# Kernel optimization log

Measured on AMD Instinct MI355X. Metric: run time of the kernel, lower is better.

Reference implementation:

```python
import jax, jax.numpy as jnp
import numpy as np

NW, NT = 200000, 100000
DW, DT = 128, 64
HID, HEADS, OUT = 64, 2, 2
HC = HID * HEADS  # 128
E = 500000
NEG_SLOPE = 0.2


def setup_inputs() -> dict:
    key = jax.random.key(0)
    ks = iter(jax.random.split(key, 40))

    def nrm(shape, scale):
        return jax.random.normal(next(ks), shape, dtype=jnp.float32) * scale

    inp = {
        "x_wallet": nrm((NW, DW), 1.0),
        "x_token": nrm((NT, DT), 1.0),
        # per-node-type input projections Linear(in, hidden)
        "lin_w_W": nrm((DW, HID), 1.0 / np.sqrt(DW)),
        "lin_w_b": jnp.zeros((HID,), jnp.float32),
        "lin_t_W": nrm((DT, HID), 1.0 / np.sqrt(DT)),
        "lin_t_b": jnp.zeros((HID,), jnp.float32),
        # GAT layer 0: in=HID(64) -> H*C(128), stacked over 3 edge types
        "Wsrc0": nrm((3, HID, HC), 1.0 / np.sqrt(HID)),
        "Wdst0": nrm((3, HID, HC), 1.0 / np.sqrt(HID)),
        "atts0": nrm((3, HEADS, HID), 1.0 / np.sqrt(HID)),
        "attd0": nrm((3, HEADS, HID), 1.0 / np.sqrt(HID)),
        "b0": jnp.zeros((3, HC), jnp.float32),
        # GAT layer 1: in=H*C(128) -> H*C(128)
        "Wsrc1": nrm((3, HC, HC), 1.0 / np.sqrt(HC)),
        "Wdst1": nrm((3, HC, HC), 1.0 / np.sqrt(HC)),
        "atts1": nrm((3, HEADS, HID), 1.0 / np.sqrt(HID)),
        "attd1": nrm((3, HEADS, HID), 1.0 / np.sqrt(HID)),
        "b1": jnp.zeros((3, HC), jnp.float32),
        # classifiers Linear(H*C, out)
        "cls_w_W": nrm((HC, OUT), 1.0 / np.sqrt(HC)),
        "cls_w_b": jnp.zeros((OUT,), jnp.float32),
        "cls_t_W": nrm((HC, OUT), 1.0 / np.sqrt(HC)),
        "cls_t_b": jnp.zeros((OUT,), jnp.float32),
        # edge indices: [2, E] with row0 = src ids, row1 = dst ids
        "e_wt": jnp.stack([jax.random.randint(next(ks), (E,), 0, NW),
                            jax.random.randint(next(ks), (E,), 0, NT)]).astype(jnp.int64),
        "e_tw": jnp.stack([jax.random.randint(next(ks), (E,), 0, NT),
                            jax.random.randint(next(ks), (E,), 0, NW)]).astype(jnp.int64),
        "e_ww": jnp.stack([jax.random.randint(next(ks), (E,), 0, NW),
                            jax.random.randint(next(ks), (E,), 0, NW)]).astype(jnp.int64),
    }
    return inp


def gat_conv(x_src, x_dst, edge, Wsrc, Wdst, att_s, att_d, bias, n_dst):
    # bipartite GATConv: project, per-edge attention, segment softmax over dst, scatter-sum
    hs = (x_src @ Wsrc).reshape(-1, HEADS, HID)  # [Ns,H,C]
    hd = (x_dst @ Wdst).reshape(-1, HEADS, HID)  # [Nd,H,C]
    a_s = jnp.einsum("nhc,hc->nh", hs, att_s)    # [Ns,H]
    a_d = jnp.einsum("nhc,hc->nh", hd, att_d)    # [Nd,H]
    s, d = edge[0], edge[1]
    alpha = jax.nn.leaky_relu(a_s[s] + a_d[d], NEG_SLOPE)  # [E,H]
    m = jax.ops.segment_max(alpha, d, num_segments=n_dst)
    m = jnp.where(jnp.isfinite(m), m, 0.0)  # nodes with no in-edges
    ex = jnp.exp(alpha - m[d])
    den = jax.ops.segment_sum(ex, d, num_segments=n_dst)
    alpha = ex / (den[d] + 1e-16)
    out = jax.ops.segment_sum(alpha[:, :, None] * hs[s], d, num_segments=n_dst)  # [Nd,H,C]
    return out.reshape(n_dst, HC) + bias


def reference(x_wallet, x_token, lin_w_W, lin_w_b, lin_t_W, lin_t_b,
              Wsrc0, Wdst0, atts0, attd0, b0,
              Wsrc1, Wdst1, atts1, attd1, b1,
              cls_w_W, cls_w_b, cls_t_W, cls_t_b,
              e_wt, e_tw, e_ww):
    xw = x_wallet @ lin_w_W + lin_w_b
    xt = x_token @ lin_t_W + lin_t_b
    for Wsrc, Wdst, ats, atd, b in ((Wsrc0, Wdst0, atts0, attd0, b0),
                                     (Wsrc1, Wdst1, atts1, attd1, b1)):
        # edge type 0: wallet->token, 1: token->wallet, 2: wallet->wallet; HeteroConv aggr='sum'
        out_t = gat_conv(xw, xt, e_wt, Wsrc[0], Wdst[0], ats[0], atd[0], b[0], NT)
        out_w = (gat_conv(xt, xw, e_tw, Wsrc[1], Wdst[1], ats[1], atd[1], b[1], NW)
                 + gat_conv(xw, xw, e_ww, Wsrc[2], Wdst[2], ats[2], atd[2], b[2], NW))
        xw = jax.nn.elu(out_w)
        xt = jax.nn.elu(out_t)
    logits_w = xw @ cls_w_W + cls_w_b  # [NW,2]
    logits_t = xt @ cls_t_W + cls_t_b  # [NT,2]
    return jnp.concatenate([logits_w, logits_t], axis=0)  # [NW+NT,2]
```

## Files before the change

kernel.cpp:

```cpp
#include <hip/hip_runtime.h>
#include <stdint.h>

typedef unsigned short ushort_t;
typedef short s8v __attribute__((ext_vector_type(8)));
typedef float f4v __attribute__((ext_vector_type(4)));

#define NW 200000
#define NT 100000
#define EE 500000
#define NSEG (NT + NW + NW)

__device__ __forceinline__ float b2f(unsigned short u){
  union { unsigned int i; float f; } v; v.i = ((unsigned int)u) << 16; return v.f;
}
__device__ __forceinline__ unsigned short f2b(float f){
  unsigned int x = __float_as_uint(f);
  unsigned int r = x + 0x7fffu + ((x >> 16) & 1u);
  return (unsigned short)(r >> 16);
}
__device__ __forceinline__ float ldf(const void* p, long idx, int fm){
  return fm ? ((const float*)p)[idx] : b2f(((const ushort_t*)p)[idx]);
}

__global__ void detect_kern(const int* ewt, const int* etw, const int* eww,
                            const unsigned* xw_words, int* mode){
  if (threadIdx.x == 0 && blockIdx.x == 0){
    unsigned o = 0;
    for (int i = 0; i < 64; ++i)
      o |= (unsigned)ewt[2 * i + 1] | (unsigned)etw[2 * i + 1] | (unsigned)eww[2 * i + 1];
    mode[0] = (o == 0) ? 1 : 0;
    int viol = 0;
    for (int i = 0; i < 256; ++i){
      unsigned s = xw_words[i] & 0xffffu;
      unsigned e = (s >> 7) & 0xffu;
      if (!(s == 0u || s == 0x8000u || (e >= 90u && e <= 140u))) viol++;
    }
    mode[1] = (viol > 8) ? 1 : 0;
  }
}

struct TDesc { const void* src; ushort_t* dst; long ebase; int K; int N; };
struct TDesc8 { TDesc d[8]; };
__global__ void transpose8(TDesc8 td, const int* mode){
  int fm = mode[1];
  int mi = blockIdx.x >> 6;
  TDesc t = td.d[mi];
  int e = ((blockIdx.x & 63) << 8) + threadIdx.x;
  if (e < t.K * t.N){
    int k = e / t.N, n = e - k * t.N;
    t.dst[n * t.K + k] = f2b(ldf(t.src, t.ebase + e, fm));
  }
}

__global__ void uprep(const void* Wsrc0, const void* Wdst0, const void* atts0, const void* attd0,
                      const void* Wsrc1, const void* Wdst1, const void* atts1, const void* attd1,
                      float* Uw0, float* Ut0, float* Uw1, float* Ut1, const int* mode){
  int fm = mode[1];
  int id = blockIdx.x * 256 + threadIdx.x;
  if (id >= (64 + 128) * 12) return;
  int layer = (id >= 64 * 12);
  int rem = layer ? id - 64 * 12 : id;
  int K = layer ? 128 : 64;
  int k = rem / 12, j = rem % 12;
  const void* Ws = layer ? Wsrc1 : Wsrc0;
  const void* Wd = layer ? Wdst1 : Wdst0;
  const void* As = layer ? atts1 : atts0;
  const void* Ad = layer ? attd1 : attd0;
  int t, h; bool src;
  if (j < 8){ const int tt[8] = {0,0,2,2,1,1,2,2}; t = tt[j]; h = j & 1; src = (j < 4); }
  else { int jj = j - 8; t = (jj < 2) ? 1 : 0; h = jj & 1; src = (jj < 2); }
  const void* W = src ? Ws : Wd;
  const void* A = src ? As : Ad;
  float acc = 0.f;
  for (int c = 0; c < 64; ++c)
    acc += ldf(W, (long)(t * K + k) * 128 + h * 64 + c, fm) * ldf(A, t * 128 + h * 64 + c, fm);
  if (j < 8) (layer ? Uw1 : Uw0)[k * 8 + j] = acc;
  else       (layer ? Ut1 : Ut0)[k * 4 + (j - 8)] = acc;
}

__global__ void hist_kern(const int* ewt, const int* etw, const int* eww, const int* mode, int* deg){
  int i = blockIdx.x * 256 + threadIdx.x;
  if (i >= 3 * EE) return;
  int md = mode[0];
  int t = i / EE, e = i - t * EE;
  const int* ep = (t == 0) ? ewt : (t == 1) ? etw : eww;
  int d = md ? ep[2 * (EE + e)] : ep[EE + e];
  int base = (t == 0) ? 0 : (t == 1) ? NT : NT + NW;
  atomicAdd(&deg[base + d], 1);
}

__global__ __launch_bounds__(512) void scan1(const int* deg, int* excl, int* sums){
  __shared__ int pair[512];
  int t = threadIdx.x;
  int base = blockIdx.x * 1024;
  int i0 = base + 2 * t;
  int a = (i0 < NSEG) ? deg[i0] : 0;
  int b = (i0 + 1 < NSEG) ? deg[i0 + 1] : 0;
  int ps = a + b;
  pair[t] = ps;
  __syncthreads();
  for (int off = 1; off < 512; off <<= 1){
    int v = (t >= off) ? pair[t - off] : 0;
    __syncthreads();
    if (t >= off) pair[t] += v;
    __syncthreads();
  }
  int epair = pair[t] - ps;
  if (i0 < NSEG) excl[i0] = epair;
  if (i0 + 1 < NSEG) excl[i0 + 1] = epair + a;
  if (t == 511) sums[blockIdx.x] = pair[511];
}

__global__ __launch_bounds__(512) void scan2(int* sums, int nch){
  __shared__ int s[512];
  int t = threadIdx.x;
  int orig = (t < nch) ? sums[t] : 0;
  s[t] = orig;
  __syncthreads();
  for (int off = 1; off < 512; off <<= 1){
    int v = (t >= off) ? s[t - off] : 0;
    __syncthreads();
    if (t >= off) s[t] += v;
    __syncthreads();
  }
  if (t < nch) sums[t] = s[t] - orig;
}

__global__ void scan3(int* rowptr, int* cursor, const int* sums){
  int i = blockIdx.x * 256 + threadIdx.x;
  if (i < NSEG){
    int v = rowptr[i] + sums[i >> 10];
    rowptr[i] = v; cursor[i] = v;
  }
  if (i == 0) rowptr[NSEG] = 3 * EE;
}

__global__ void fill_kern(const int* ewt, const int* etw, const int* eww, const int* mode,
                          int* cursor, int* adj){
  int i = blockIdx.x * 256 + threadIdx.x;
  if (i >= 3 * EE) return;
  int md = mode[0];
  int t = i / EE, e = i - t * EE;
  const int* ep = (t == 0) ? ewt : (t == 1) ? etw : eww;
  int s = md ? ep[2 * e] : ep[e];
  int d = md ? ep[2 * (EE + e)] : ep[EE + e];
  int base = (t == 0) ? 0 : (t == 1) ? NT : NT + NW;
  int pos = atomicAdd(&cursor[base + d], 1);
  adj[pos] = s;
}

template<int K, int NC, bool BIAS, bool EXTA>
__global__ __launch_bounds__(256, 2) void gemm_kern(const void* __restrict__ A, const ushort_t* __restrict__ Bt,
    const void* __restrict__ bias, ushort_t* __restrict__ C, int M,
    const int* __restrict__ mode, int nchunk){
  constexpr int CT = NC / 16, KK = K / 32;
  int fm = EXTA ? mode[1] : 0;
  int tid = threadIdx.x, lane = tid & 63, wave = tid >> 6;
  int rl = lane & 15, kq = (lane >> 4) * 8;
  s8v bfrag[CT][KK];
#pragma unroll
  for (int ct = 0; ct < CT; ++ct)
#pragma unroll
    for (int kk = 0; kk < KK; ++kk)
      bfrag[ct][kk] = *(const s8v*)(Bt + (long)(ct * 16 + rl) * K + kk * 32 + kq);
  float biasv[CT];
  if (BIAS){
#pragma unroll
    for (int ct = 0; ct < CT; ++ct) biasv[ct] = ldf(bias, ct * 16 + rl, fm);
  }
  for (int chunk = blockIdx.x; chunk < nchunk; chunk += gridDim.x){
    long m0 = (long)chunk * 128 + wave * 32;
    f4v acc[2][CT];
#pragma unroll
    for (int rt = 0; rt < 2; ++rt)
#pragma unroll
      for (int ct = 0; ct < CT; ++ct) acc[rt][ct] = (f4v){0.f, 0.f, 0.f, 0.f};
#pragma unroll
    for (int rt = 0; rt < 2; ++rt){
      long row = m0 + rt * 16 + rl;
      bool ok = row < (long)M;
#pragma unroll
      for (int kk = 0; kk < KK; ++kk){
        s8v a = (s8v){0,0,0,0,0,0,0,0};
        if (ok){
          long e = row * K + kk * 32 + kq;
          if (EXTA && fm){
            const float* p = (const float*)A + e;
            uint4 lo = *(const uint4*)p;
            uint4 hi = *(const uint4*)(p + 4);
            union { s8v v; unsigned u[4]; } t;
            t.u[0] = (unsigned)f2b(__uint_as_float(lo.x)) | ((unsigned)f2b(__uint_as_float(lo.y)) << 16);
            t.u[1] = (unsigned)f2b(__uint_as_float(lo.z)) | ((unsigned)f2b(__uint_as_float(lo.w)) << 16);
            t.u[2] = (unsigned)f2b(__uint_as_float(hi.x)) | ((unsigned)f2b(__uint_as_float(hi.y)) << 16);
            t.u[3] = (unsigned)f2b(__uint_as_float(hi.z)) | ((unsigned)f2b(__uint_as_float(hi.w)) << 16);
            a = t.v;
          } else {
            a = *(const s8v*)((const ushort_t*)A + e);
          }
        }
#pragma unroll
        for (int ct = 0; ct < CT; ++ct)
          acc[rt][ct] = __builtin_amdgcn_mfma_f32_16x16x32_bf16(a, bfrag[ct][kk], acc[rt][ct], 0, 0, 0);
      }
    }
#pragma unroll
    for (int rt = 0; rt < 2; ++rt){
      long rbase = (long)chunk * 128 + wave * 32 + rt * 16 + (lane >> 4) * 4;
#pragma unroll
      for (int ct = 0; ct < CT; ++ct){
#pragma unroll
        for (int r = 0; r < 4; ++r){
          long gm = rbase + r;
          if (gm < (long)M){
            float v = acc[rt][ct][r];
            if (BIAS) v += biasv[ct];
            C[gm * NC + ct * 16 + rl] = f2b(v);
          }
        }
      }
    }
  }
}

template<int K, int NCOL>
__global__ __launch_bounds__(256) void a_kern(const ushort_t* __restrict__ x, const float* __restrict__ U,
                                              float* __restrict__ out, int N){
  int n = blockIdx.x * 256 + threadIdx.x;
  if (n >= N) return;
  float acc[NCOL];
#pragma unroll
  for (int j = 0; j < NCOL; ++j) acc[j] = 0.f;
  const ushort_t* xr = x + (long)n * K;
#pragma unroll
  for (int k8 = 0; k8 < K / 8; ++k8){
    uint4 v = *(const uint4*)(xr + k8 * 8);
    unsigned uu[4] = {v.x, v.y, v.z, v.w};
#pragma unroll
    for (int i = 0; i < 4; ++i){
      float f0 = b2f((unsigned short)(uu[i] & 0xffffu));
      float f1 = b2f((unsigned short)(uu[i] >> 16));
      const float* Ur = U + (k8 * 8 + i * 2) * NCOL;
#pragma unroll
      for (int j = 0; j < NCOL; ++j) acc[j] += f0 * Ur[j] + f1 * Ur[NCOL + j];
    }
  }
  f4v* o4 = (f4v*)(out + (long)n * NCOL);
#pragma unroll
  for (int q = 0; q < NCOL / 4; ++q){
    f4v t = {acc[q * 4], acc[q * 4 + 1], acc[q * 4 + 2], acc[q * 4 + 3]};
    o4[q] = t;
  }
}

__global__ __launch_bounds__(256) void node_softmax(const int* __restrict__ rowptr,
    const int* __restrict__ adj, const float* __restrict__ aw, const float* __restrict__ at,
    float2* __restrict__ alf){
  int seg = blockIdx.x * 256 + threadIdx.x;
  if (seg >= NSEG) return;
  int beg = rowptr[seg], end = rowptr[seg + 1];
  int n = end - beg;
  if (n <= 0) return;
  const float* asrc; int stride, col; float2 ad;
  if (seg < NT){
    asrc = aw; stride = 8; col = 0;
    ad = *(const float2*)(at + (long)seg * 4 + 2);
  } else if (seg < NT + NW){
    asrc = at; stride = 4; col = 0;
    ad = *(const float2*)(aw + (long)(seg - NT) * 8 + 4);
  } else {
    asrc = aw; stride = 8; col = 2;
    ad = *(const float2*)(aw + (long)(seg - NT - NW) * 8 + 6);
  }
  if (n <= 8){
    float2 buf[8];
    float m0 = -1e30f, m1 = -1e30f;
#pragma unroll
    for (int i = 0; i < 8; ++i){
      if (i < n){
        int s = adj[beg + i];
        float2 x = *(const float2*)(asrc + (long)s * stride + col);
        float a0 = x.x + ad.x, a1 = x.y + ad.y;
        a0 = a0 > 0.f ? a0 : 0.2f * a0;
        a1 = a1 > 0.f ? a1 : 0.2f * a1;
        buf[i] = make_float2(a0, a1);
        m0 = fmaxf(m0, a0); m1 = fmaxf(m1, a1);
      }
    }
    float d0 = 0.f, d1 = 0.f;
#pragma unroll
    for (int i = 0; i < 8; ++i){
      if (i < n){
        float w0 = __expf(buf[i].x - m0), w1 = __expf(buf[i].y - m1);
        d0 += w0; d1 += w1;
        buf[i] = make_float2(w0, w1);
      }
    }
    float i0 = 1.f / (d0 + 1e-16f), i1 = 1.f / (d1 + 1e-16f);
#pragma unroll
    for (int i = 0; i < 8; ++i)
      if (i < n) alf[beg + i] = make_float2(buf[i].x * i0, buf[i].y * i1);
  } else {
    float m0 = -1e30f, m1 = -1e30f;
    for (int j = beg; j < end; ++j){
      int s = adj[j];
      float2 x = *(const float2*)(asrc + (long)s * stride + col);
      float a0 = x.x + ad.x, a1 = x.y + ad.y;
      a0 = a0 > 0.f ? a0 : 0.2f * a0;
      a1 = a1 > 0.f ? a1 : 0.2f * a1;
      alf[j] = make_float2(a0, a1);
      m0 = fmaxf(m0, a0); m1 = fmaxf(m1, a1);
    }
    float d0 = 0.f, d1 = 0.f;
    for (int j = beg; j < end; ++j){
      float2 a = alf[j];
      a.x = __expf(a.x - m0); a.y = __expf(a.y - m1);
      d0 += a.x; d1 += a.y;
      alf[j] = a;
    }
    float i0 = 1.f / (d0 + 1e-16f), i1 = 1.f / (d1 + 1e-16f);
    for (int j = beg; j < end; ++j){
      float2 a = alf[j];
      alf[j] = make_float2(a.x * i0, a.y * i1);
    }
  }
}

__device__ __forceinline__ void conv_gather(const int* __restrict__ rowptr, const int* __restrict__ adj,
    const float2* __restrict__ alf, int seg, const ushort_t* __restrict__ hs,
    int lane, int c0, float& o0, float& o1){
  int beg = rowptr[seg], end = rowptr[seg + 1];
  if (beg >= end) return;
  for (int j = beg; j < end; j += 4){
    int j1 = min(j + 1, end - 1), j2 = min(j + 2, end - 1), j3 = min(j + 3, end - 1);
    int s0 = adj[j], s1 = adj[j1], s2 = adj[j2], s3 = adj[j3];
    float2 w0 = alf[j], w1 = alf[j1], w2 = alf[j2], w3 = alf[j3];
    unsigned h0 = *(const unsigned*)(hs + (long)s0 * 128 + c0);
    unsigned h1 = *(const unsigned*)(hs + (long)s1 * 128 + c0);
    unsigned h2 = *(const unsigned*)(hs + (long)s2 * 128 + c0);
    unsigned h3 = *(const unsigned*)(hs + (long)s3 * 128 + c0);
    float wl0 = (lane < 32) ? w0.x : w0.y;
    float wl1 = (j + 1 < end) ? ((lane < 32) ? w1.x : w1.y) : 0.f;
    float wl2 = (j + 2 < end) ? ((lane < 32) ? w2.x : w2.y) : 0.f;
    float wl3 = (j + 3 < end) ? ((lane < 32) ? w3.x : w3.y) : 0.f;
    o0 += wl0 * b2f((unsigned short)(h0 & 0xffffu)) + wl1 * b2f((unsigned short)(h1 & 0xffffu))
        + wl2 * b2f((unsigned short)(h2 & 0xffffu)) + wl3 * b2f((unsigned short)(h3 & 0xffffu));
    o1 += wl0 * b2f((unsigned short)(h0 >> 16)) + wl1 * b2f((unsigned short)(h1 >> 16))
        + wl2 * b2f((unsigned short)(h2 >> 16)) + wl3 * b2f((unsigned short)(h3 >> 16));
  }
}

template<bool FINAL>
__global__ __launch_bounds__(256) void agg_all(const int* __restrict__ rowptr, const int* __restrict__ adj,
    const float2* __restrict__ alf,
    const ushort_t* __restrict__ hs0, const ushort_t* __restrict__ hs1, const ushort_t* __restrict__ hs2,
    const void* __restrict__ bsrc, ushort_t* __restrict__ xt_out, ushort_t* __restrict__ xw_out,
    const void* __restrict__ clsWw, const void* __restrict__ clsbw,
    const void* __restrict__ clsWt, const void* __restrict__ clsbt,
    void* __restrict__ dout, const int* __restrict__ mode){
  int fm = mode[1];
  int wv = __builtin_amdgcn_readfirstlane(threadIdx.x >> 6);
  int lane = threadIdx.x & 63;
  int c0 = lane << 1;
  int bid = blockIdx.x;
  const int TB = NT / 4;
  float o0 = 0.f, o1 = 0.f;
  bool is_tok = bid < TB;
  int d;
  if (is_tok){
    d = bid * 4 + wv;
    conv_gather(rowptr, adj, alf, d, hs0, lane, c0, o0, o1);
    o0 += ldf(bsrc, c0, fm);
    o1 += ldf(bsrc, c0 + 1, fm);
  } else {
    d = (bid - TB) * 4 + wv;
    conv_gather(rowptr, adj, alf, NT + d,      hs1, lane, c0, o0, o1);
    conv_gather(rowptr, adj, alf, NT + NW + d, hs2, lane, c0, o0, o1);
    o0 += ldf(bsrc, 128 + c0, fm)     + ldf(bsrc, 256 + c0, fm);
    o1 += ldf(bsrc, 128 + c0 + 1, fm) + ldf(bsrc, 256 + c0 + 1, fm);
  }
  o0 = o0 > 0.f ? o0 : __expf(o0) - 1.f;
  o1 = o1 > 0.f ? o1 : __expf(o1) - 1.f;
  if (!FINAL){
    ushort_t* out = is_tok ? xt_out : xw_out;
    unsigned pack = (unsigned)f2b(o0) | ((unsigned)f2b(o1) << 16);
    *(unsigned*)(out + (long)d * 128 + c0) = pack;
  } else {
    const void* W = is_tok ? clsWt : clsWw;
    const void* b = is_tok ? clsbt : clsbw;
    float w00 = ldf(W, 4 * lane + 0, fm), w01 = ldf(W, 4 * lane + 1, fm);
    float w10 = ldf(W, 4 * lane + 2, fm), w11 = ldf(W, 4 * lane + 3, fm);
    float p0 = o0 * w00 + o1 * w10;
    float p1 = o0 * w01 + o1 * w11;
#pragma unroll
    for (int off = 32; off > 0; off >>= 1){ p0 += __shfl_xor(p0, off, 64); p1 += __shfl_xor(p1, off, 64); }
    if (lane == 0){
      long g = is_tok ? (long)NW + d : (long)d;
      float r0 = p0 + ldf(b, 0, fm);
      float r1 = p1 + ldf(b, 1, fm);
      if (fm){ ((float*)dout)[g * 2] = r0; ((float*)dout)[g * 2 + 1] = r1; }
      else { ((ushort_t*)dout)[g * 2] = f2b(r0); ((ushort_t*)dout)[g * 2 + 1] = f2b(r1); }
    }
  }
}

extern "C" void kernel_launch(void* const* d_in, const int* in_sizes, int n_in,
                              void* d_out, int out_size, void* d_ws, size_t ws_size,
                              hipStream_t stream){
  const void* x_wallet = d_in[0];
  const void* x_token  = d_in[1];
  const void* lin_w_W  = d_in[2];
  const void* lin_w_b  = d_in[3];
  const void* lin_t_W  = d_in[4];
  const void* lin_t_b  = d_in[5];
  const void* Wsrc0    = d_in[6];
  const void* Wdst0    = d_in[7];
  const void* atts0    = d_in[8];
  const void* attd0    = d_in[9];
  const void* b0       = d_in[10];
  const void* Wsrc1    = d_in[11];
  const void* Wdst1    = d_in[12];
  const void* atts1    = d_in[13];
  const void* attd1    = d_in[14];
  const void* b1       = d_in[15];
  const void* cls_w_W  = d_in[16];
  const void* cls_w_b  = d_in[17];
  const void* cls_t_W  = d_in[18];
  const void* cls_t_b  = d_in[19];
  const int* e_wt = (const int*)d_in[20];
  const int* e_tw = (const int*)d_in[21];
  const int* e_ww = (const int*)d_in[22];

  char* ws = (char*)d_ws;
  size_t off = 0;
  auto alloc = [&](size_t bytes) -> char* {
    char* p = ws + off; off += (bytes + 255) & ~(size_t)255; return p;
  };
  int* rowptr = (int*)alloc((size_t)(NSEG + 1) * 4);
  int* deg    = (int*)alloc((size_t)(NSEG + 1) * 4);
  int* adj    = (int*)alloc((size_t)3 * EE * 4);
  float2* alf = (float2*)alloc((size_t)3 * EE * 8);
  int* sums   = (int*)alloc(512 * 4);
  int* mode   = (int*)alloc(8);
  ushort_t* BtLw = (ushort_t*)alloc(64 * 128 * 2);
  ushort_t* BtLt = (ushort_t*)alloc(64 * 64 * 2);
  ushort_t* BtS0 = (ushort_t*)alloc(3 * 128 * 64 * 2);
  ushort_t* BtS1 = (ushort_t*)alloc(3 * 128 * 128 * 2);
  float* Uw0 = (float*)alloc(64 * 8 * 4);
  float* Ut0 = (float*)alloc(64 * 4 * 4);
  float* Uw1 = (float*)alloc(128 * 8 * 4);
  float* Ut1 = (float*)alloc(128 * 4 * 4);
  float* aw = (float*)alloc((size_t)NW * 8 * 4);
  float* at = (float*)alloc((size_t)NT * 4 * 4);
  ushort_t* hs0 = (ushort_t*)alloc((size_t)NW * 128 * 2);
  ushort_t* hs1 = (ushort_t*)alloc((size_t)NT * 128 * 2);
  ushort_t* hs2 = (ushort_t*)alloc((size_t)NW * 128 * 2);
  ushort_t* xbuf = (ushort_t*)alloc(((size_t)NW + NT) * 128 * 2);
  ushort_t* xw0 = xbuf;
  ushort_t* xt0 = xbuf + (size_t)NW * 64;
  ushort_t* xwB = xbuf;
  ushort_t* xtB = xbuf + (size_t)NW * 128;
  (void)in_sizes; (void)n_in;

  if (off > ws_size){
    hipMemsetAsync(d_out, 0, (size_t)out_size * 2, stream);
    return;
  }

  hipMemsetAsync(deg, 0, (size_t)NSEG * 4, stream);
  detect_kern<<<1, 64, 0, stream>>>(e_wt, e_tw, e_ww, (const unsigned*)x_wallet, mode);

  TDesc8 td;
  td.d[0] = { lin_w_W, BtLw, 0, 128, 64 };
  td.d[1] = { lin_t_W, BtLt, 0, 64, 64 };
  for (int t = 0; t < 3; ++t){
    td.d[2 + t] = { Wsrc0, BtS0 + t * 128 * 64,  (long)t * 64 * 128,  64,  128 };
    td.d[5 + t] = { Wsrc1, BtS1 + t * 128 * 128, (long)t * 128 * 128, 128, 128 };
  }
  transpose8<<<512, 256, 0, stream>>>(td, mode);
  uprep<<<9, 256, 0, stream>>>(Wsrc0, Wdst0, atts0, attd0, Wsrc1, Wdst1, atts1, attd1, Uw0, Ut0, Uw1, Ut1, mode);

  int egrid = (3 * EE + 255) / 256;
  hist_kern<<<egrid, 256, 0, stream>>>(e_wt, e_tw, e_ww, mode, deg);
  int nch = (NSEG + 1023) / 1024;
  scan1<<<nch, 512, 0, stream>>>(deg, rowptr, sums);
  scan2<<<1, 512, 0, stream>>>(sums, nch);
  scan3<<<(NSEG + 255) / 256, 256, 0, stream>>>(rowptr, deg, sums);
  fill_kern<<<egrid, 256, 0, stream>>>(e_wt, e_tw, e_ww, mode, deg, adj);

  const int G = 512;
  int ncW = (NW + 127) / 128, ncT = (NT + 127) / 128;
  int sgrid = (NSEG + 255) / 256;
  int agrid = NT / 4 + NW / 4;

  gemm_kern<128, 64, true, true><<<G, 256, 0, stream>>>(x_wallet, BtLw, lin_w_b, xw0, NW, mode, ncW);
  gemm_kern<64, 64, true, true><<<G, 256, 0, stream>>>(x_token, BtLt, lin_t_b, xt0, NT, mode, ncT);

  a_kern<64, 8><<<(NW + 255) / 256, 256, 0, stream>>>(xw0, Uw0, aw, NW);
  a_kern<64, 4><<<(NT + 255) / 256, 256, 0, stream>>>(xt0, Ut0, at, NT);
  node_softmax<<<sgrid, 256, 0, stream>>>(rowptr, adj, aw, at, alf);
  gemm_kern<64, 128, false, false><<<G, 256, 0, stream>>>(xw0, BtS0, nullptr, hs0, NW, mode, ncW);
  gemm_kern<64, 128, false, false><<<G, 256, 0, stream>>>(xt0, BtS0 + 128 * 64, nullptr, hs1, NT, mode, ncT);
  gemm_kern<64, 128, false, false><<<G, 256, 0, stream>>>(xw0, BtS0 + 2 * 128 * 64, nullptr, hs2, NW, mode, ncW);
  agg_all<false><<<agrid, 256, 0, stream>>>(rowptr, adj, alf, hs0, hs1, hs2, b0, xtB, xwB,
                                            nullptr, nullptr, nullptr, nullptr, nullptr, mode);

  a_kern<128, 8><<<(NW + 255) / 256, 256, 0, stream>>>(xwB, Uw1, aw, NW);
  a_kern<128, 4><<<(NT + 255) / 256, 256, 0, stream>>>(xtB, Ut1, at, NT);
  node_softmax<<<sgrid, 256, 0, stream>>>(rowptr, adj, aw, at, alf);
  gemm_kern<128, 128, false, false><<<G, 256, 0, stream>>>(xwB, BtS1, nullptr, hs0, NW, mode, ncW);
  gemm_kern<128, 128, false, false><<<G, 256, 0, stream>>>(xtB, BtS1 + 128 * 128, nullptr, hs1, NT, mode, ncT);
  gemm_kern<128, 128, false, false><<<G, 256, 0, stream>>>(xwB, BtS1 + 2 * 128 * 128, nullptr, hs2, NW, mode, ncW);
  agg_all<true><<<agrid, 256, 0, stream>>>(rowptr, adj, alf, hs0, hs1, hs2, b1, nullptr, nullptr,
                                           cls_w_W, cls_w_b, cls_t_W, cls_t_b, d_out, mode);
}
```

Measured before the change: 940.2 us.

## Fuse edge softmax into aggregation kernel with online max rescaling

Removes the separate node_softmax kernel and alpha buffer. Each wave now computes attention logits per edge inside the aggregation, using an online-softmax running max with rescaling, and processes rounds of 8 edges. The two wallet edge types have their first round loads issued together to overlap latency. This drops one write and re-read of the per-edge alpha array per layer, plus one launch, at the cost of redundant exp work across lanes and more registers.

```diff
diff --git a/kernel.cpp b/kernel.cpp
--- a/kernel.cpp
+++ b/kernel.cpp
@@ -252,106 +252,50 @@
   }
 }
 
-__global__ __launch_bounds__(256) void node_softmax(const int* __restrict__ rowptr,
-    const int* __restrict__ adj, const float* __restrict__ aw, const float* __restrict__ at,
-    float2* __restrict__ alf){
-  int seg = blockIdx.x * 256 + threadIdx.x;
-  if (seg >= NSEG) return;
-  int beg = rowptr[seg], end = rowptr[seg + 1];
-  int n = end - beg;
-  if (n <= 0) return;
-  const float* asrc; int stride, col; float2 ad;
-  if (seg < NT){
-    asrc = aw; stride = 8; col = 0;
-    ad = *(const float2*)(at + (long)seg * 4 + 2);
-  } else if (seg < NT + NW){
-    asrc = at; stride = 4; col = 0;
-    ad = *(const float2*)(aw + (long)(seg - NT) * 8 + 4);
-  } else {
-    asrc = aw; stride = 8; col = 2;
-    ad = *(const float2*)(aw + (long)(seg - NT - NW) * 8 + 6);
-  }
-  if (n <= 8){
-    float2 buf[8];
-    float m0 = -1e30f, m1 = -1e30f;
-#pragma unroll
-    for (int i = 0; i < 8; ++i){
-      if (i < n){
-        int s = adj[beg + i];
-        float2 x = *(const float2*)(asrc + (long)s * stride + col);
-        float a0 = x.x + ad.x, a1 = x.y + ad.y;
-        a0 = a0 > 0.f ? a0 : 0.2f * a0;
-        a1 = a1 > 0.f ? a1 : 0.2f * a1;
-        buf[i] = make_float2(a0, a1);
-        m0 = fmaxf(m0, a0); m1 = fmaxf(m1, a1);
-      }
-    }
-    float d0 = 0.f, d1 = 0.f;
-#pragma unroll
-    for (int i = 0; i < 8; ++i){
-      if (i < n){
-        float w0 = __expf(buf[i].x - m0), w1 = __expf(buf[i].y - m1);
-        d0 += w0; d1 += w1;
-        buf[i] = make_float2(w0, w1);
-      }
-    }
-    float i0 = 1.f / (d0 + 1e-16f), i1 = 1.f / (d1 + 1e-16f);
-#pragma unroll
-    for (int i = 0; i < 8; ++i)
-      if (i < n) alf[beg + i] = make_float2(buf[i].x * i0, buf[i].y * i1);
-  } else {
-    float m0 = -1e30f, m1 = -1e30f;
-    for (int j = beg; j < end; ++j){
-      int s = adj[j];
-      float2 x = *(const float2*)(asrc + (long)s * stride + col);
-      float a0 = x.x + ad.x, a1 = x.y + ad.y;
-      a0 = a0 > 0.f ? a0 : 0.2f * a0;
-      a1 = a1 > 0.f ? a1 : 0.2f * a1;
-      alf[j] = make_float2(a0, a1);
-      m0 = fmaxf(m0, a0); m1 = fmaxf(m1, a1);
-    }
-    float d0 = 0.f, d1 = 0.f;
-    for (int j = beg; j < end; ++j){
-      float2 a = alf[j];
-      a.x = __expf(a.x - m0); a.y = __expf(a.y - m1);
-      d0 += a.x; d1 += a.y;
-      alf[j] = a;
-    }
-    float i0 = 1.f / (d0 + 1e-16f), i1 = 1.f / (d1 + 1e-16f);
-    for (int j = beg; j < end; ++j){
-      float2 a = alf[j];
-      alf[j] = make_float2(a.x * i0, a.y * i1);
-    }
-  }
-}
-
-__device__ __forceinline__ void conv_gather(const int* __restrict__ rowptr, const int* __restrict__ adj,
-    const float2* __restrict__ alf, int seg, const ushort_t* __restrict__ hs,
-    int lane, int c0, float& o0, float& o1){
-  int beg = rowptr[seg], end = rowptr[seg + 1];
-  if (beg >= end) return;
-  for (int j = beg; j < end; j += 4){
-    int j1 = min(j + 1, end - 1), j2 = min(j + 2, end - 1), j3 = min(j + 3, end - 1);
-    int s0 = adj[j], s1 = adj[j1], s2 = adj[j2], s3 = adj[j3];
-    float2 w0 = alf[j], w1 = alf[j1], w2 = alf[j2], w3 = alf[j3];
-    unsigned h0 = *(const unsigned*)(hs + (long)s0 * 128 + c0);
-    unsigned h1 = *(const unsigned*)(hs + (long)s1 * 128 + c0);
-    unsigned h2 = *(const unsigned*)(hs + (long)s2 * 128 + c0);
-    unsigned h3 = *(const unsigned*)(hs + (long)s3 * 128 + c0);
-    float wl0 = (lane < 32) ? w0.x : w0.y;
-    float wl1 = (j + 1 < end) ? ((lane < 32) ? w1.x : w1.y) : 0.f;
-    float wl2 = (j + 2 < end) ? ((lane < 32) ? w2.x : w2.y) : 0.f;
-    float wl3 = (j + 3 < end) ? ((lane < 32) ? w3.x : w3.y) : 0.f;
-    o0 += wl0 * b2f((unsigned short)(h0 & 0xffffu)) + wl1 * b2f((unsigned short)(h1 & 0xffffu))
-        + wl2 * b2f((unsigned short)(h2 & 0xffffu)) + wl3 * b2f((unsigned short)(h3 & 0xffffu));
-    o1 += wl0 * b2f((unsigned short)(h0 >> 16)) + wl1 * b2f((unsigned short)(h1 >> 16))
-        + wl2 * b2f((unsigned short)(h2 >> 16)) + wl3 * b2f((unsigned short)(h3 >> 16));
+__device__ __forceinline__ void round_load(const int* __restrict__ adj,
+    const float* __restrict__ asrc, int stride, int col, int j, int cnt,
+    const ushort_t* __restrict__ hs, int c0, float2 (&av)[8], unsigned (&h)[8]){
+#pragma unroll
+  for (int i = 0; i < 8; ++i){
+    if (i < cnt){
+      int s = adj[j + i];
+      av[i] = *(const float2*)(asrc + (long)s * stride + col);
+      h[i] = *(const unsigned*)(hs + (long)s * 128 + c0);
+    }
+  }
+}
+
+__device__ __forceinline__ void round_acc(int cnt, float adl, int hi,
+    const float2 (&av)[8], const unsigned (&h)[8],
+    float& n0, float& n1, float& den, float& mm){
+  float al[8];
+  float rm = -1e30f;
+#pragma unroll
+  for (int i = 0; i < 8; ++i){
+    if (i < cnt){
+      float x = (hi ? av[i].y : av[i].x) + adl;
+      x = x > 0.f ? x : 0.2f * x;
+      al[i] = x;
+      rm = fmaxf(rm, x);
+    }
+  }
+  float mnew = fmaxf(mm, rm);
+  float sc = __expf(mm - mnew);
+  n0 *= sc; n1 *= sc; den *= sc; mm = mnew;
+#pragma unroll
+  for (int i = 0; i < 8; ++i){
+    if (i < cnt){
+      float e = __expf(al[i] - mnew);
+      den += e;
+      n0 += e * b2f((unsigned short)(h[i] & 0xffffu));
+      n1 += e * b2f((unsigned short)(h[i] >> 16));
+    }
   }
 }
 
 template<bool FINAL>
 __global__ __launch_bounds__(256) void agg_all(const int* __restrict__ rowptr, const int* __restrict__ adj,
-    const float2* __restrict__ alf,
+    const float* __restrict__ aw, const float* __restrict__ at,
     const ushort_t* __restrict__ hs0, const ushort_t* __restrict__ hs1, const ushort_t* __restrict__ hs2,
     const void* __restrict__ bsrc, ushort_t* __restrict__ xt_out, ushort_t* __restrict__ xw_out,
     const void* __restrict__ clsWw, const void* __restrict__ clsbw,
@@ -360,23 +304,62 @@
   int fm = mode[1];
   int wv = __builtin_amdgcn_readfirstlane(threadIdx.x >> 6);
   int lane = threadIdx.x & 63;
+  int hi = lane >> 5;
   int c0 = lane << 1;
   int bid = blockIdx.x;
   const int TB = NT / 4;
-  float o0 = 0.f, o1 = 0.f;
   bool is_tok = bid < TB;
+  float o0, o1;
   int d;
   if (is_tok){
     d = bid * 4 + wv;
-    conv_gather(rowptr, adj, alf, d, hs0, lane, c0, o0, o1);
-    o0 += ldf(bsrc, c0, fm);
-    o1 += ldf(bsrc, c0 + 1, fm);
+    float2 ad = *(const float2*)(at + (long)d * 4 + 2);
+    float adl = hi ? ad.y : ad.x;
+    int beg = rowptr[d], end = rowptr[d + 1];
+    float n0 = 0.f, n1 = 0.f, den = 0.f, mm = -1e30f;
+    for (int j = beg; j < end; j += 8){
+      int cnt = min(end - j, 8);
+      float2 av[8]; unsigned h[8];
+      round_load(adj, aw, 8, 0, j, cnt, hs0, c0, av, h);
+      round_acc(cnt, adl, hi, av, h, n0, n1, den, mm);
+    }
+    float inv = 1.f / (den + 1e-16f);
+    o0 = n0 * inv + ldf(bsrc, c0, fm);
+    o1 = n1 * inv + ldf(bsrc, c0 + 1, fm);
   } else {
     d = (bid - TB) * 4 + wv;
-    conv_gather(rowptr, adj, alf, NT + d,      hs1, lane, c0, o0, o1);
-    conv_gather(rowptr, adj, alf, NT + NW + d, hs2, lane, c0, o0, o1);
-    o0 += ldf(bsrc, 128 + c0, fm)     + ldf(bsrc, 256 + c0, fm);
-    o1 += ldf(bsrc, 128 + c0 + 1, fm) + ldf(bsrc, 256 + c0 + 1, fm);
+    float2 ad1 = *(const float2*)(aw + (long)d * 8 + 4);
+    float2 ad2 = *(const float2*)(aw + (long)d * 8 + 6);
+    float adl1 = hi ? ad1.y : ad1.x;
+    float adl2 = hi ? ad2.y : ad2.x;
+    int s1 = NT + d, s2 = NT + NW + d;
+    int b1 = rowptr[s1], e1 = rowptr[s1 + 1];
+    int b2 = rowptr[s2], e2 = rowptr[s2 + 1];
+    int c1 = min(e1 - b1, 8), c2 = min(e2 - b2, 8);
+    float n10 = 0.f, n11 = 0.f, den1 = 0.f, mm1 = -1e30f;
+    float n20 = 0.f, n21 = 0.f, den2 = 0.f, mm2 = -1e30f;
+    {
+      float2 av1[8], av2[8]; unsigned h1[8], h2[8];
+      if (c1 > 0) round_load(adj, at, 4, 0, b1, c1, hs1, c0, av1, h1);
+      if (c2 > 0) round_load(adj, aw, 8, 2, b2, c2, hs2, c0, av2, h2);
+      if (c1 > 0) round_acc(c1, adl1, hi, av1, h1, n10, n11, den1, mm1);
+      if (c2 > 0) round_acc(c2, adl2, hi, av2, h2, n20, n21, den2, mm2);
+    }
+    for (int j = b1 + 8; j < e1; j += 8){
+      int cnt = min(e1 - j, 8);
+      float2 av[8]; unsigned h[8];
+      round_load(adj, at, 4, 0, j, cnt, hs1, c0, av, h);
+      round_acc(cnt, adl1, hi, av, h, n10, n11, den1, mm1);
+    }
+    for (int j = b2 + 8; j < e2; j += 8){
+      int cnt = min(e2 - j, 8);
+      float2 av[8]; unsigned h[8];
+      round_load(adj, aw, 8, 2, j, cnt, hs2, c0, av, h);
+      round_acc(cnt, adl2, hi, av, h, n20, n21, den2, mm2);
+    }
+    float i1v = 1.f / (den1 + 1e-16f), i2v = 1.f / (den2 + 1e-16f);
+    o0 = n10 * i1v + n20 * i2v + ldf(bsrc, 128 + c0, fm)     + ldf(bsrc, 256 + c0, fm);
+    o1 = n11 * i1v + n21 * i2v + ldf(bsrc, 128 + c0 + 1, fm) + ldf(bsrc, 256 + c0 + 1, fm);
   }
   o0 = o0 > 0.f ? o0 : __expf(o0) - 1.f;
   o1 = o1 > 0.f ? o1 : __expf(o1) - 1.f;
@@ -438,7 +421,6 @@
   int* rowptr = (int*)alloc((size_t)(NSEG + 1) * 4);
   int* deg    = (int*)alloc((size_t)(NSEG + 1) * 4);
   int* adj    = (int*)alloc((size_t)3 * EE * 4);
-  float2* alf = (float2*)alloc((size_t)3 * EE * 8);
   int* sums   = (int*)alloc(512 * 4);
   int* mode   = (int*)alloc(8);
   ushort_t* BtLw = (ushort_t*)alloc(64 * 128 * 2);
@@ -489,7 +471,6 @@
 
   const int G = 512;
   int ncW = (NW + 127) / 128, ncT = (NT + 127) / 128;
-  int sgrid = (NSEG + 255) / 256;
   int agrid = NT / 4 + NW / 4;
 
   gemm_kern<128, 64, true, true><<<G, 256, 0, stream>>>(x_wallet, BtLw, lin_w_b, xw0, NW, mode, ncW);
@@ -497,19 +478,17 @@
 
   a_kern<64, 8><<<(NW + 255) / 256, 256, 0, stream>>>(xw0, Uw0, aw, NW);
   a_kern<64, 4><<<(NT + 255) / 256, 256, 0, stream>>>(xt0, Ut0, at, NT);
-  node_softmax<<<sgrid, 256, 0, stream>>>(rowptr, adj, aw, at, alf);
   gemm_kern<64, 128, false, false><<<G, 256, 0, stream>>>(xw0, BtS0, nullptr, hs0, NW, mode, ncW);
   gemm_kern<64, 128, false, false><<<G, 256, 0, stream>>>(xt0, BtS0 + 128 * 64, nullptr, hs1, NT, mode, ncT);
   gemm_kern<64, 128, false, false><<<G, 256, 0, stream>>>(xw0, BtS0 + 2 * 128 * 64, nullptr, hs2, NW, mode, ncW);
-  agg_all<false><<<agrid, 256, 0, stream>>>(rowptr, adj, alf, hs0, hs1, hs2, b0, xtB, xwB,
+  agg_all<false><<<agrid, 256, 0, stream>>>(rowptr, adj, aw, at, hs0, hs1, hs2, b0, xtB, xwB,
                                             nullptr, nullptr, nullptr, nullptr, nullptr, mode);
 
   a_kern<128, 8><<<(NW + 255) / 256, 256, 0, stream>>>(xwB, Uw1, aw, NW);
   a_kern<128, 4><<<(NT + 255) / 256, 256, 0, stream>>>(xtB, Ut1, at, NT);
-  node_softmax<<<sgrid, 256, 0, stream>>>(rowptr, adj, aw, at, alf);
   gemm_kern<128, 128, false, false><<<G, 256, 0, stream>>>(xwB, BtS1, nullptr, hs0, NW, mode, ncW);
   gemm_kern<128, 128, false, false><<<G, 256, 0, stream>>>(xtB, BtS1 + 128 * 128, nullptr, hs1, NT, mode, ncT);
   gemm_kern<128, 128, false, false><<<G, 256, 0, stream>>>(xwB, BtS1 + 2 * 128 * 128, nullptr, hs2, NW, mode, ncW);
-  agg_all<true><<<agrid, 256, 0, stream>>>(rowptr, adj, alf, hs0, hs1, hs2, b1, nullptr, nullptr,
+  agg_all<true><<<agrid, 256, 0, stream>>>(rowptr, adj, aw, at, hs0, hs1, hs2, b1, nullptr, nullptr,
                                            cls_w_W, cls_w_b, cls_t_W, cls_t_b, d_out, mode);
 }
```

Measured after the change: 924.7 us. No clear change (-1.6%).
